# Optimization experiments

Measured on AMD Instinct MI355X. Metric: run time of the kernel, lower is better.

Reference implementation:

```python
import jax, jax.numpy as jnp
import numpy as np

NUM_ITERATIONS = 3


def squash(s, axis=-1):
    # v = (|s|^2 / (1+|s|^2)) * s / |s|  (standard CapsNet squash)
    sq_norm = jnp.sum(s * s, axis=axis, keepdims=True)
    return (sq_norm / (1.0 + sq_norm)) * s / jnp.sqrt(sq_norm + 1e-9)


def setup_inputs() -> dict:
    key = jax.random.key(0)
    k1, k2 = jax.random.split(key)
    B, IN_C, OUT_C, OUT_D, IN_D = 64, 2048, 32, 16, 8
    x = jax.random.normal(k1, (B, IN_C, IN_D), dtype=jnp.float32)
    W = jax.random.normal(k2, (1, IN_C, OUT_C, OUT_D, IN_D), dtype=jnp.float32)
    return {"x": x, "W": W}


def reference(x, W):
    # u_hat[b,i,o,d] = sum_m W[0,i,o,d,m] * x[b,i,m]
    u_hat = jnp.einsum('iodm,bim->biod', W[0], x)  # [B, IN_C, OUT_C, OUT_D]
    B, IN_C, OUT_C, _ = u_hat.shape
    b_logits = jnp.zeros((B, IN_C, OUT_C), dtype=u_hat.dtype)
    v = None
    for _ in range(NUM_ITERATIONS):
        # PyTorch F.softmax(b) with implicit dim=1 for a 4-D tensor -> softmax over in_channels
        c = jax.nn.softmax(b_logits, axis=1)               # [B, IN_C, OUT_C]
        s = jnp.einsum('bio,biod->bod', c, u_hat)          # [B, OUT_C, OUT_D]
        v = squash(s)                                      # [B, OUT_C, OUT_D]
        b_logits = b_logits + jnp.einsum('biod,bod->bio', u_hat, v)
    return v
```

## Files before the change

### kernel.cpp

```cpp
#include <hip/hip_runtime.h>
#include <math.h>

#define B_ 64
#define IC 2048
#define OC 32
#define OD 16
#define ID 8

typedef __attribute__((ext_vector_type(8)))  short s16x8;
typedef __attribute__((ext_vector_type(16))) float f32x16;

__device__ __forceinline__ unsigned short f2bf(float f) {
  unsigned u = __float_as_uint(f);
  return (unsigned short)((u + 0x7fffu + ((u >> 16) & 1u)) >> 16);
}
__device__ __forceinline__ float bf2f(unsigned short h) {
  return __uint_as_float(((unsigned)h) << 16);
}
__device__ __forceinline__ f32x16 mfma16(s16x8 a, s16x8 b, f32x16 c) {
  return __builtin_amdgcn_mfma_f32_32x32x16_bf16(a, b, c, 0, 0, 0);
}

__global__ __launch_bounds__(256) void convWX(
    const float* __restrict__ W, const float* __restrict__ x,
    unsigned short* __restrict__ Wbf, unsigned short* __restrict__ xb)
{
  const int bid = blockIdx.x;
  if (bid < 8192) {
    const int e4 = bid * 256 + threadIdx.x;
    const float4 v = ((const float4*)W)[e4];
    const int i = e4 >> 10;
    const int r = (e4 & 1023) << 2;
    ushort4 h, l;
    h.x = f2bf(v.x); l.x = f2bf(v.x - bf2f(h.x));
    h.y = f2bf(v.y); l.y = f2bf(v.y - bf2f(h.y));
    h.z = f2bf(v.z); l.z = f2bf(v.z - bf2f(h.z));
    h.w = f2bf(v.w); l.w = f2bf(v.w - bf2f(h.w));
    *(ushort4*)&Wbf[(size_t)i * 8192 + r]        = h;
    *(ushort4*)&Wbf[(size_t)i * 8192 + 4096 + r] = l;
  } else {
    const int idx = (bid - 8192) * 256 + threadIdx.x;
    const int m2 = idx & 1, i = (idx >> 1) & 2047, b = idx >> 12;
    const float4 v = *(const float4*)(x + (size_t)b * 16384 + i * 8 + m2 * 4);
    ushort4 h, l;
    h.x = f2bf(v.x); l.x = f2bf(v.x - bf2f(h.x));
    h.y = f2bf(v.y); l.y = f2bf(v.y - bf2f(h.y));
    h.z = f2bf(v.z); l.z = f2bf(v.z - bf2f(h.z));
    h.w = f2bf(v.w); l.w = f2bf(v.w - bf2f(h.w));
    *(ushort4*)&xb[(size_t)i * 1024 + b * 8 + m2 * 4]       = h;
    *(ushort4*)&xb[(size_t)i * 1024 + 512 + b * 8 + m2 * 4] = l;
  }
}

template<bool WEIGHTED, int NCH>
__global__ __launch_bounds__(256) void fusedM(
    const unsigned short* __restrict__ Wbf, const unsigned short* __restrict__ xb,
    const float* __restrict__ vss, float* __restrict__ part,
    float* __restrict__ zpart)
{
  constexpr int CI = IC / NCH;
  const int t     = threadIdx.x;
  const int ch    = blockIdx.x % NCH;
  const int q     = blockIdx.x / NCH;
  const int lane  = t & 63;
  const int wv    = t >> 6;
  const int s     = q * 4 + wv;
  const int opair = s >> 1;
  const int bt    = s & 1;
  const int l31   = lane & 31;
  const int hb    = lane >> 5;
  const int i0    = ch * CI;

  const unsigned short* ap =
      Wbf + (size_t)i0 * 8192 + opair * 256 + (l31 >> 4) * 128 + (lane & 15) * 8;
  const unsigned short* bp =
      xb + (size_t)i0 * 1024 + hb * 512 + bt * 256 + l31 * 8;

  f32x16 acc = (f32x16)0.0f;
  float zA = 0.f, zB = 0.f;
  float vsr[16];

  if constexpr (WEIGHTED) {
    const float* vp = vss + s * 1024 + hb * 32 + l31;
#pragma unroll
    for (int r = 0; r < 16; ++r) vsr[r] = vp[r * 64];
  }

  s16x8 AH[3], AL[3], BV[3];
  AH[0] = *(const s16x8*)ap;
  AL[0] = *(const s16x8*)(ap + 4096);
  BV[0] = *(const s16x8*)bp;
  if (CI > 1) {
    AH[1] = *(const s16x8*)(ap + 8192);
    AL[1] = *(const s16x8*)(ap + 8192 + 4096);
    BV[1] = *(const s16x8*)(bp + 1024);
  }

#pragma unroll
  for (int ii = 0; ii < CI; ++ii) {
    const int cs = ii % 3;
    const int ns = (ii + 2) % 3;
    if (ii + 2 < CI) {
      AH[ns] = *(const s16x8*)(ap + (size_t)(ii + 2) * 8192);
      AL[ns] = *(const s16x8*)(ap + (size_t)(ii + 2) * 8192 + 4096);
      BV[ns] = *(const s16x8*)(bp + (size_t)(ii + 2) * 1024);
    }

    if constexpr (!WEIGHTED) {
      acc = mfma16(AH[cs], BV[cs], acc);
      acc = mfma16(AL[cs], BV[cs], acc);
    } else {
      f32x16 u = mfma16(AH[cs], BV[cs], (f32x16)0.0f);
      u = mfma16(AL[cs], BV[cs], u);
      float pdA = 0.f, pdB = 0.f;
#pragma unroll
      for (int r = 0; r < 8; ++r)  pdA = fmaf(u[r], vsr[r], pdA);
#pragma unroll
      for (int r = 8; r < 16; ++r) pdB = fmaf(u[r], vsr[r], pdB);
      pdA += __shfl_xor(pdA, 32);
      pdB += __shfl_xor(pdB, 32);
      const float pA = __expf(pdA), pB = __expf(pdB);
#pragma unroll
      for (int r = 0; r < 8; ++r)  acc[r] = fmaf(pA, u[r], acc[r]);
#pragma unroll
      for (int r = 8; r < 16; ++r) acc[r] = fmaf(pB, u[r], acc[r]);
      zA += pA; zB += pB;
    }
  }

  float* op = part + (size_t)ch * 32768;
#pragma unroll
  for (int r = 0; r < 16; ++r)
    op[(s * 16 + r) * 64 + hb * 32 + l31] = acc[r];
  if constexpr (WEIGHTED) {
    if (lane < 32) {
      zpart[(size_t)ch * 2048 + (s * 2 + 0) * 32 + lane] = zA;
      zpart[(size_t)ch * 2048 + (s * 2 + 1) * 32 + lane] = zB;
    }
  }
}

template<bool WEIGHTED, int NCH>
__global__ __launch_bounds__(512) void rsqA(
    const float* __restrict__ part, const float* __restrict__ zpart,
    float* __restrict__ pp2, float* __restrict__ zp2)
{
  constexpr int CPG = NCH / 16;
  const int t  = threadIdx.x;
  const int g  = blockIdx.x >> 6;
  const int sl = blockIdx.x & 63;
  const size_t tid = (size_t)sl * 512 + t;

  float acc = 0.f;
#pragma unroll 8
  for (int c = 0; c < CPG; ++c)
    acc += part[(size_t)(g * CPG + c) * 32768 + tid];
  pp2[(size_t)g * 32768 + tid] = acc;

  if constexpr (WEIGHTED) {
    if (sl == 0) {
#pragma unroll
      for (int k = 0; k < 4; ++k) {
        const int j = t + 512 * k;
        float zs = 0.f;
#pragma unroll 8
        for (int c = 0; c < CPG; ++c)
          zs += zpart[(size_t)(g * CPG + c) * 2048 + j];
        zp2[(size_t)g * 2048 + j] = zs;
      }
    }
  }
}

template<int PASS>
__global__ __launch_bounds__(512) void rsqB(
    const float* __restrict__ pp2, const float* __restrict__ zp2,
    float* __restrict__ vss, float* __restrict__ out)
{
  __shared__ float rzs[32];
  __shared__ float sqs[512];
  const int t   = threadIdx.x;
  const int blk = blockIdx.x;
  const int s   = blk >> 1, oo = blk & 1;
  const int l31 = t & 31, hb = (t >> 5) & 1, rr = t >> 6;
  const size_t tid = (size_t)blk * 512 + t;

  float acc = 0.f;
#pragma unroll
  for (int g = 0; g < 16; ++g) acc += pp2[(size_t)g * 32768 + tid];

  if constexpr (PASS == 0) {
    if (t < 32) rzs[t] = 1.f / 2048.f;
  } else {
    if (t < 32) {
      float zs = 0.f;
#pragma unroll
      for (int g = 0; g < 16; ++g)
        zs += zp2[(size_t)g * 2048 + (s * 2 + oo) * 32 + t];
      rzs[t] = 1.f / zs;
    }
  }
  __syncthreads();
  const float sv = acc * rzs[l31];
  sqs[t] = sv * sv;
  __syncthreads();
  float sq = 0.f;
#pragma unroll
  for (int k = 0; k < 16; ++k) sq += sqs[l31 + k * 32];
  const float f = (sq / (1.f + sq)) * rsqrtf(sq + 1e-9f);
  const float v = sv * f;

  if constexpr (PASS == 0)      vss[tid] = v;
  else if constexpr (PASS == 1) vss[tid] += v;
  else {
    const int b = (s & 1) * 32 + l31;
    const int o = (s >> 1) * 2 + oo;
    const int d = (rr & 3) + 8 * (rr >> 2) + 4 * hb;
    out[(b * 32 + o) * 16 + d] = v;
  }
}

template<int PASS, int NCH>
__global__ __launch_bounds__(512) void rsqM(
    const float* __restrict__ part, const float* __restrict__ zpart,
    float* __restrict__ vss, float* __restrict__ out)
{
  __shared__ float rzs[32];
  __shared__ float sqs[512];
  const int t   = threadIdx.x;
  const int blk = blockIdx.x;
  const int s   = blk >> 1, oo = blk & 1;
  const int l31 = t & 31, hb = (t >> 5) & 1, rr = t >> 6;
  const size_t tid = (size_t)blk * 512 + t;

  float acc = 0.f;
#pragma unroll 8
  for (int ch = 0; ch < NCH; ++ch) acc += part[(size_t)ch * 32768 + tid];

  if constexpr (PASS == 0) {
    if (t < 32) rzs[t] = 1.f / 2048.f;
  } else {
    if (t < 32) {
      float zs = 0.f;
#pragma unroll 8
      for (int ch = 0; ch < NCH; ++ch)
        zs += zpart[(size_t)ch * 2048 + (s * 2 + oo) * 32 + t];
      rzs[t] = 1.f / zs;
    }
  }
  __syncthreads();
  const float sv = acc * rzs[l31];
  sqs[t] = sv * sv;
  __syncthreads();
  float sq = 0.f;
#pragma unroll
  for (int k = 0; k < 16; ++k) sq += sqs[l31 + k * 32];
  const float f = (sq / (1.f + sq)) * rsqrtf(sq + 1e-9f);
  const float v = sv * f;

  if constexpr (PASS == 0)      vss[tid] = v;
  else if constexpr (PASS == 1) vss[tid] += v;
  else {
    const int b = (s & 1) * 32 + l31;
    const int o = (s >> 1) * 2 + oo;
    const int d = (rr & 3) + 8 * (rr >> 2) + 4 * hb;
    out[(b * 32 + o) * 16 + d] = v;
  }
}

extern "C" void kernel_launch(void* const* d_in, const int* in_sizes, int n_in,
                              void* d_out, int out_size, void* d_ws, size_t ws_size,
                              hipStream_t stream) {
  (void)in_sizes; (void)n_in; (void)out_size;
  const float* x = (const float*)d_in[0];
  const float* W = (const float*)d_in[1];
  float* out = (float*)d_out;
  float* ws  = (float*)d_ws;

  const size_t WBF_US = (size_t)IC * 8192;
  const size_t XB_US  = (size_t)IC * 1024;

  const size_t need256 =
      ((size_t)256 * 32768 + 256ul * 2048 + 16ul * 32768 + 16ul * 2048 + 32768) * 4
      + (WBF_US + XB_US) * 2;
  const size_t need128 =
      ((size_t)128 * 32768 + 128ul * 2048 + 32768) * 4 + (WBF_US + XB_US) * 2;

  if (ws_size >= need256) {
    constexpr int NCH = 256;
    float* part  = ws;
    float* zpart = part + (size_t)NCH * 32768;
    float* pp2   = zpart + (size_t)NCH * 2048;
    float* zp2   = pp2 + 16ul * 32768;
    float* vsb   = zp2 + 16ul * 2048;
    unsigned short* Wbf = (unsigned short*)(vsb + 32768);
    unsigned short* xbp = Wbf + WBF_US;

    const dim3 b256(256), b512(512), gF(8 * NCH), gA(1024), gB(64);
    convWX<<<dim3(9216), b256, 0, stream>>>(W, x, Wbf, xbp);
    fusedM<false, NCH><<<gF, b256, 0, stream>>>(Wbf, xbp, nullptr, part, nullptr);
    rsqA<false, NCH><<<gA, b512, 0, stream>>>(part, nullptr, pp2, nullptr);
    rsqB<0><<<gB, b512, 0, stream>>>(pp2, nullptr, vsb, nullptr);
    fusedM<true, NCH><<<gF, b256, 0, stream>>>(Wbf, xbp, vsb, part, zpart);
    rsqA<true, NCH><<<gA, b512, 0, stream>>>(part, zpart, pp2, zp2);
    rsqB<1><<<gB, b512, 0, stream>>>(pp2, zp2, vsb, nullptr);
    fusedM<true, NCH><<<gF, b256, 0, stream>>>(Wbf, xbp, vsb, part, zpart);
    rsqA<true, NCH><<<gA, b512, 0, stream>>>(part, zpart, pp2, zp2);
    rsqB<2><<<gB, b512, 0, stream>>>(pp2, zp2, nullptr, out);
    return;
  }

  {
    constexpr int NCH = 128;
    float* part  = ws;
    float* zpart = part + (size_t)NCH * 32768;
    float* vsb   = zpart + (size_t)NCH * 2048;
    unsigned short* Wbf = (unsigned short*)(vsb + 32768);
    unsigned short* xbp = Wbf + WBF_US;
    (void)need128;

    const dim3 b256(256), b512(512), gF(8 * NCH), gR(64);
    convWX<<<dim3(9216), b256, 0, stream>>>(W, x, Wbf, xbp);
    fusedM<false, NCH><<<gF, b256, 0, stream>>>(Wbf, xbp, nullptr, part, nullptr);
    rsqM<0, NCH><<<gR, b512, 0, stream>>>(part, nullptr, vsb, nullptr);
    fusedM<true, NCH><<<gF, b256, 0, stream>>>(Wbf, xbp, vsb, part, zpart);
    rsqM<1, NCH><<<gR, b512, 0, stream>>>(part, zpart, vsb, nullptr);
    fusedM<true, NCH><<<gF, b256, 0, stream>>>(Wbf, xbp, vsb, part, zpart);
    rsqM<2, NCH><<<gR, b512, 0, stream>>>(part, zpart, nullptr, out);
  }
}
```

Baseline: 100.8 us.

## Drop 256-chunk two-stage reduction path in favor of 128-chunk single-stage path

```diff
diff --git a/kernel.cpp b/kernel.cpp
--- a/kernel.cpp
+++ b/kernel.cpp
@@ -140,86 +140,6 @@
   }
 }
 
-template<bool WEIGHTED, int NCH>
-__global__ __launch_bounds__(512) void rsqA(
-    const float* __restrict__ part, const float* __restrict__ zpart,
-    float* __restrict__ pp2, float* __restrict__ zp2)
-{
-  constexpr int CPG = NCH / 16;
-  const int t  = threadIdx.x;
-  const int g  = blockIdx.x >> 6;
-  const int sl = blockIdx.x & 63;
-  const size_t tid = (size_t)sl * 512 + t;
-
-  float acc = 0.f;
-#pragma unroll 8
-  for (int c = 0; c < CPG; ++c)
-    acc += part[(size_t)(g * CPG + c) * 32768 + tid];
-  pp2[(size_t)g * 32768 + tid] = acc;
-
-  if constexpr (WEIGHTED) {
-    if (sl == 0) {
-#pragma unroll
-      for (int k = 0; k < 4; ++k) {
-        const int j = t + 512 * k;
-        float zs = 0.f;
-#pragma unroll 8
-        for (int c = 0; c < CPG; ++c)
-          zs += zpart[(size_t)(g * CPG + c) * 2048 + j];
-        zp2[(size_t)g * 2048 + j] = zs;
-      }
-    }
-  }
-}
-
-template<int PASS>
-__global__ __launch_bounds__(512) void rsqB(
-    const float* __restrict__ pp2, const float* __restrict__ zp2,
-    float* __restrict__ vss, float* __restrict__ out)
-{
-  __shared__ float rzs[32];
-  __shared__ float sqs[512];
-  const int t   = threadIdx.x;
-  const int blk = blockIdx.x;
-  const int s   = blk >> 1, oo = blk & 1;
-  const int l31 = t & 31, hb = (t >> 5) & 1, rr = t >> 6;
-  const size_t tid = (size_t)blk * 512 + t;
-
-  float acc = 0.f;
-#pragma unroll
-  for (int g = 0; g < 16; ++g) acc += pp2[(size_t)g * 32768 + tid];
-
-  if constexpr (PASS == 0) {
-    if (t < 32) rzs[t] = 1.f / 2048.f;
-  } else {
-    if (t < 32) {
-      float zs = 0.f;
-#pragma unroll
-      for (int g = 0; g < 16; ++g)
-        zs += zp2[(size_t)g * 2048 + (s * 2 + oo) * 32 + t];
-      rzs[t] = 1.f / zs;
-    }
-  }
-  __syncthreads();
-  const float sv = acc * rzs[l31];
-  sqs[t] = sv * sv;
-  __syncthreads();
-  float sq = 0.f;
-#pragma unroll
-  for (int k = 0; k < 16; ++k) sq += sqs[l31 + k * 32];
-  const float f = (sq / (1.f + sq)) * rsqrtf(sq + 1e-9f);
-  const float v = sv * f;
-
-  if constexpr (PASS == 0)      vss[tid] = v;
-  else if constexpr (PASS == 1) vss[tid] += v;
-  else {
-    const int b = (s & 1) * 32 + l31;
-    const int o = (s >> 1) * 2 + oo;
-    const int d = (rr & 3) + 8 * (rr >> 2) + 4 * hb;
-    out[(b * 32 + o) * 16 + d] = v;
-  }
-}
-
 template<int PASS, int NCH>
 __global__ __launch_bounds__(512) void rsqM(
     const float* __restrict__ part, const float* __restrict__ zpart,
@@ -280,44 +200,13 @@
   const size_t WBF_US = (size_t)IC * 8192;
   const size_t XB_US  = (size_t)IC * 1024;
 
-  const size_t need256 =
-      ((size_t)256 * 32768 + 256ul * 2048 + 16ul * 32768 + 16ul * 2048 + 32768) * 4
-      + (WBF_US + XB_US) * 2;
-  const size_t need128 =
-      ((size_t)128 * 32768 + 128ul * 2048 + 32768) * 4 + (WBF_US + XB_US) * 2;
-
-  if (ws_size >= need256) {
-    constexpr int NCH = 256;
-    float* part  = ws;
-    float* zpart = part + (size_t)NCH * 32768;
-    float* pp2   = zpart + (size_t)NCH * 2048;
-    float* zp2   = pp2 + 16ul * 32768;
-    float* vsb   = zp2 + 16ul * 2048;
-    unsigned short* Wbf = (unsigned short*)(vsb + 32768);
-    unsigned short* xbp = Wbf + WBF_US;
-
-    const dim3 b256(256), b512(512), gF(8 * NCH), gA(1024), gB(64);
-    convWX<<<dim3(9216), b256, 0, stream>>>(W, x, Wbf, xbp);
-    fusedM<false, NCH><<<gF, b256, 0, stream>>>(Wbf, xbp, nullptr, part, nullptr);
-    rsqA<false, NCH><<<gA, b512, 0, stream>>>(part, nullptr, pp2, nullptr);
-    rsqB<0><<<gB, b512, 0, stream>>>(pp2, nullptr, vsb, nullptr);
-    fusedM<true, NCH><<<gF, b256, 0, stream>>>(Wbf, xbp, vsb, part, zpart);
-    rsqA<true, NCH><<<gA, b512, 0, stream>>>(part, zpart, pp2, zp2);
-    rsqB<1><<<gB, b512, 0, stream>>>(pp2, zp2, vsb, nullptr);
-    fusedM<true, NCH><<<gF, b256, 0, stream>>>(Wbf, xbp, vsb, part, zpart);
-    rsqA<true, NCH><<<gA, b512, 0, stream>>>(part, zpart, pp2, zp2);
-    rsqB<2><<<gB, b512, 0, stream>>>(pp2, zp2, nullptr, out);
-    return;
-  }
-
-  {
-    constexpr int NCH = 128;
+  auto runM = [&](auto tag) {
+    constexpr int NCH = decltype(tag)::value;
     float* part  = ws;
     float* zpart = part + (size_t)NCH * 32768;
     float* vsb   = zpart + (size_t)NCH * 2048;
     unsigned short* Wbf = (unsigned short*)(vsb + 32768);
     unsigned short* xbp = Wbf + WBF_US;
-    (void)need128;
 
     const dim3 b256(256), b512(512), gF(8 * NCH), gR(64);
     convWX<<<dim3(9216), b256, 0, stream>>>(W, x, Wbf, xbp);
@@ -327,5 +216,14 @@
     rsqM<1, NCH><<<gR, b512, 0, stream>>>(part, zpart, vsb, nullptr);
     fusedM<true, NCH><<<gF, b256, 0, stream>>>(Wbf, xbp, vsb, part, zpart);
     rsqM<2, NCH><<<gR, b512, 0, stream>>>(part, zpart, nullptr, out);
-  }
-}
+  };
+
+  const size_t need128 =
+      ((size_t)128 * 32768 + 128ul * 2048 + 32768) * 4 + (WBF_US + XB_US) * 2;
+  const size_t need64 =
+      ((size_t)64 * 32768 + 64ul * 2048 + 32768) * 4 + (WBF_US + XB_US) * 2;
+  (void)need64;
+
+  if (ws_size >= need128) runM(std::integral_constant<int, 128>{});
+  else                    runM(std::integral_constant<int, 64>{});
+}
```

New measurement: 95.48 us. 5.3% less time.
